# Optimization experiments

Hardware: AMD Instinct MI355X
Metric: run time of the kernel (lower is better)

## Reference

```python
import jax, jax.numpy as jnp
import numpy as np

N, TAPS, DIMS = 100000, 32, 2
LR_W, LR_F, LR_S, LR_B = 1.0 / 2**4, 1.0 / 2**7, 0.0, 1.0 / 2**11
GRAD_MAX_W, GRAD_MAX_F = 30.0, 30.0
EPS = 1e-8
BETA = 0.0  # commplax ddlms default: fshat <- f * s each step


def qam16_const():
    a = np.array([-3.0, -1.0, 1.0, 3.0], dtype=np.float32)
    re, im = np.meshgrid(a, a)
    c = (re + 1j * im).reshape(-1).astype(np.complex64)
    c = c / np.sqrt(np.mean(np.abs(c) ** 2))  # unit average power (/= sqrt(10))
    return jnp.asarray(c, dtype=jnp.complex64)


def mimo(w, u):
    # w: [dims, dims, taps], u: [taps, dims] -> [dims]
    return jnp.einsum('ijt,tj->i', w, u)


def setup_inputs() -> dict:
    key = jax.random.key(0)
    framed_signal_ri = jax.random.normal(key, (N, TAPS, DIMS, 2), dtype=jnp.float32)
    return {"framed_signal_ri": framed_signal_ri}


def reference(framed_signal_ri):
    u_all = (framed_signal_ri[..., 0] + 1j * framed_signal_ri[..., 1]).astype(jnp.complex64)  # [N, taps, dims]
    const = qam16_const()

    w0 = jnp.zeros((DIMS, DIMS, TAPS), jnp.complex64)
    f0 = jnp.ones((DIMS,), jnp.complex64)
    s0 = jnp.ones((DIMS,), jnp.complex64)
    b0 = jnp.zeros((DIMS,), jnp.complex64)
    fshat0 = jnp.ones((DIMS,), jnp.complex64)

    def clip_cmplx(g, gmax):
        # |g|<=gmax: unchanged; else g/|g|*gmax. Safe form (no div-by-zero).
        return g * (gmax / jnp.maximum(jnp.abs(g), gmax))

    def step(carry, u):
        w, f, s, b, fshat = carry
        v = mimo(w, u)                 # [dims]
        k = v * f
        c = k * s
        z = c + b
        q = v * fshat + b
        # decision-directed symbol (train=False)
        d = jax.lax.stop_gradient(const[jnp.argmin(jnp.abs(const[:, None] - q[None, :]), axis=0)])
        l = jnp.sum(jnp.abs(z - d) ** 2)

        psi_hat = jnp.abs(f) / f * jnp.abs(s) / s
        e_w = (d - b) * psi_hat - v
        e_f = d - b - k
        e_s = d - b - c
        e_b = d - z
        gw = (-1.0 / (jnp.sum(jnp.abs(u) ** 2) + EPS)) * e_w[:, None, None] * jnp.conj(u).T[None, ...]
        gf = (-1.0 / (jnp.abs(v) ** 2 + EPS)) * e_f * jnp.conj(v)
        gs = (-1.0 / (jnp.abs(k) ** 2 + EPS)) * e_s * jnp.conj(k)
        gb = -e_b

        gw = clip_cmplx(gw, GRAD_MAX_W)
        gf = clip_cmplx(gf, GRAD_MAX_F)

        out = ((w, f, s, b), l)  # weights used at this step + loss

        w = w - LR_W * gw
        f = f - LR_F * gf
        s = s - LR_S * gs
        b = b - LR_B * gb
        fshat = BETA * fshat + (1.0 - BETA) * (f * s)
        return (w, f, s, b, fshat), out

    _, ((ws, fs, ss, bs), ls) = jax.lax.scan(step, (w0, f0, s0, b0, fshat0), u_all)
    # apply: per-step equalization with the step's weights
    signal = jax.vmap(mimo)(ws, u_all) * fs * ss + bs   # [N, dims] complex64
    # emit as real/imag float32 pair for harness comparability
    return jnp.stack([jnp.real(signal), jnp.imag(signal)], axis=-1)
```

## Files before the change

kernel.cpp:

```cpp
#include <hip/hip_runtime.h>

#define N_STEPS 100000
#define NDIMS 2
#define ELEMS 64
#define LR_W 0.0625f
#define LR_F 0.0078125f
#define LR_B 0.00048828125f
#define GMAXF 30.0f
#define EPS_C 1e-8f
#define C_HALF_S10 1.58113883f
#define INV_S10 0.316227766f
#define TWO_INV_S10 0.6324555320f

#define DPPADD(v, ctrl, rmask)                                                   \
    do {                                                                         \
        int _t = __builtin_amdgcn_update_dpp(0, __float_as_int(v), ctrl, rmask,  \
                                             0xF, true);                         \
        (v) += __int_as_float(_t);                                               \
    } while (0)

__device__ inline float allsum64(float x) {
    x += __shfl_xor(x, 1);
    x += __shfl_xor(x, 2);
    x += __shfl_xor(x, 4);
    x += __shfl_xor(x, 8);
    x += __shfl_xor(x, 16);
    x += __shfl_xor(x, 32);
    return x;
}

__global__ __launch_bounds__(256) void ddlms_pre(const float2* __restrict__ u,
                                                 float4* __restrict__ C,
                                                 float2* __restrict__ D) {
    const int wave = threadIdx.x >> 6;
    const int lane = threadIdx.x & 63;
    const int n = blockIdx.x * 4 + wave;
    if (n >= N_STEPS) return;
    const int n1 = min(n + 1, N_STEPS - 1);
    const int n2 = min(n + 2, N_STEPS - 1);
    float2 u0 = u[(size_t)n  * ELEMS + lane];
    float2 u1 = u[(size_t)n1 * ELEMS + lane];
    float2 u2 = u[(size_t)n2 * ELEMS + lane];
    float su  = u0.x * u0.x + u0.y * u0.y;
    float r1r = u0.x * u1.x + u0.y * u1.y;
    float r1i = u0.x * u1.y - u0.y * u1.x;
    float r2r = u0.x * u2.x + u0.y * u2.y;
    float r2i = u0.x * u2.y - u0.y * u2.x;
    su  = allsum64(su);
    r1r = allsum64(r1r);
    r1i = allsum64(r1i);
    r2r = allsum64(r2r);
    r2i = allsum64(r2i);
    if (lane == 0) {
        float kappa = LR_W / (su + EPS_C);
        C[n] = make_float4(kappa, kappa * r1r, kappa * r1i, 0.0f);
        D[n] = make_float2(kappa * r2r, kappa * r2i);
    }
}

__global__ __launch_bounds__(64, 1) void ddlms_main(const float2* __restrict__ uin,
                                                    const float4* __restrict__ C,
                                                    const float2* __restrict__ D,
                                                    float2* __restrict__ out) {
    const int dim  = blockIdx.x;
    const int lane = threadIdx.x;

    float wr = 0.0f, wi = 0.0f;
    float vr = 0.0f, vi = 0.0f;
    float fr = 1.0f, fi = 0.0f;
    float br = 0.0f, bi = 0.0f;
    float psir = 1.0f, psii = 0.0f;
    float fs2r = C_HALF_S10, fs2i = 0.0f;
    float bs2r = 0.0f, bs2i = 0.0f;
    float nbr = -INV_S10, nbi = -INV_S10;
    float redr = 0.0f, redi = 0.0f;
    float vpr = 0.0f, vpi = 0.0f;

    float2 ubuf[8];
    float2 uc = uin[lane];
#pragma unroll
    for (int k = 1; k <= 8; ++k)
        ubuf[k & 7] = uin[(size_t)k * ELEMS + lane];

    float4 creg[4];
    float2 dreg[4];
#pragma unroll
    for (int k = 0; k < 4; ++k) {
        creg[k] = C[k];
        dreg[k] = D[k];
    }

    float2 zbuf[8];
    float2* outp = out + dim;

    for (int nb = 0; nb < N_STEPS; nb += 8) {
#pragma unroll
        for (int q = 0; q < 8; ++q) {
            const int n = nb + q;

            const float kap = creg[q & 3].x;
            const float k1r = creg[q & 3].y;
            const float k1i = creg[q & 3].z;
            const float k2r = dreg[q & 3].x;
            const float k2i = dreg[q & 3].y;
            {
                const int cn = min(n + 4, N_STEPS - 1);
                creg[q & 3] = C[cn];
                dreg[q & 3] = D[cn];
            }

            float P2r = redr, P2i = redi;
            DPPADD(P2r, 0x140, 0xF); DPPADD(P2i, 0x140, 0xF);
            DPPADD(P2r, 0x142, 0xA); DPPADD(P2i, 0x142, 0xA);
            DPPADD(P2r, 0x143, 0xC); DPPADD(P2i, 0x143, 0xC);
            const float sP2r = __int_as_float(__builtin_amdgcn_readlane(__float_as_int(P2r), 63));
            const float sP2i = __int_as_float(__builtin_amdgcn_readlane(__float_as_int(P2i), 63));

            const float2 u2 = ubuf[(q + 2) & 7];
            float pr = fmaf(wr, u2.x, -wi * u2.y);
            float pi = fmaf(wr, u2.y,  wi * u2.x);
            DPPADD(pr, 0xB1, 0xF);  DPPADD(pi, 0xB1, 0xF);
            DPPADD(pr, 0x4E, 0xF);  DPPADD(pi, 0x4E, 0xF);
            DPPADD(pr, 0x141, 0xF); DPPADD(pi, 0x141, 0xF);

            const float2 un = ubuf[(q + 1) & 7];
            ubuf[(q + 1) & 7] = uin[(size_t)min(n + 9, N_STEPS - 1) * ELEMS + lane];

            const float m2v  = fmaf(vr, vr, vi * vi);
            const float me   = m2v + EPS_C;
            const float invv = __builtin_amdgcn_rcpf(me);
            const float LFi  = LR_F * invv;
            const float Gme  = GMAXF * me;

            const float zr = fmaf(vr, fr, fmaf(-vi, fi, br));
            const float zi = fmaf(vr, fi, fmaf( vi, fr, bi));
            zbuf[q] = make_float2(zr, zi);

            const float zsr = fmaf(vr, fs2r, fmaf(-vi, fs2i, bs2r));
            const float zsi = fmaf(vr, fs2i, fmaf( vi, fs2r, bs2i));
            const float mr = __builtin_amdgcn_fmed3f(ceilf(zsr), -1.0f, 2.0f);
            const float mi = __builtin_amdgcn_fmed3f(ceilf(zsi), -1.0f, 2.0f);

            const float dbr = fmaf(TWO_INV_S10, mr, nbr);
            const float dbi = fmaf(TWO_INV_S10, mi, nbi);
            const float er  = fmaf(TWO_INV_S10, mr, -(INV_S10 + zr));
            const float ei  = fmaf(TWO_INV_S10, mi, -(INV_S10 + zi));

            const float ewr = fmaf(dbr, psir, fmaf(-dbi, psii, -vr));
            const float ewi = fmaf(dbr, psii, fmaf( dbi, psir, -vi));

            const float baser = sP2r + vpr;
            const float basei = sP2i + vpi;
            const float vnr = fmaf(k1r, ewr, fmaf(-k1i, ewi, baser));
            const float vni = fmaf(k1r, ewi, fmaf( k1i, ewr, basei));

            vpr = fmaf(k2r, ewr, -k2i * ewi);
            vpi = fmaf(k2r, ewi,  k2i * ewr);

            const float mwr = kap * ewr, mwi = kap * ewi;
            wr = fmaf(mwr, uc.x, fmaf( mwi, uc.y, wr));
            wi = fmaf(mwi, uc.x, fmaf(-mwr, uc.y, wi));

            const float e2  = fmaf(er, er, ei * ei);
            const float rs  = __builtin_amdgcn_rsqf(e2 * m2v);
            const float fac = fminf(1.0f, Gme * rs);
            const float s   = LFi * fac;
            const float ecvr = fmaf(er, vr,  ei * vi);
            const float ecvi = fmaf(ei, vr, -er * vi);
            fr = fmaf(s, ecvr, fr);
            fi = fmaf(s, ecvi, fi);

            br = fmaf(LR_B, er, br);
            bi = fmaf(LR_B, ei, bi);

            const float m2f = fmaf(fr, fr, fi * fi);
            const float rsf = __builtin_amdgcn_rsqf(m2f);
            psir = fr * rsf;
            psii = -fi * rsf;

            fs2r = C_HALF_S10 * fr; fs2i = C_HALF_S10 * fi;
            bs2r = C_HALF_S10 * br; bs2i = C_HALF_S10 * bi;
            nbr = -(INV_S10 + br);  nbi = -(INV_S10 + bi);

            vr = vnr; vi = vni;
            uc = un;
            redr = pr; redi = pi;
        }

        if (lane == 0) {
#pragma unroll
            for (int q = 0; q < 8; ++q)
                outp[(size_t)(nb + q) * NDIMS] = zbuf[q];
        }
    }
}

extern "C" void kernel_launch(void* const* d_in, const int* in_sizes, int n_in,
                              void* d_out, int out_size, void* d_ws, size_t ws_size,
                              hipStream_t stream) {
    const float2* u = (const float2*)d_in[0];
    float4* C = (float4*)d_ws;
    float2* D = (float2*)((char*)d_ws + (size_t)N_STEPS * sizeof(float4));
    ddlms_pre<<<(N_STEPS + 3) / 4, 256, 0, stream>>>(u, C, D);
    ddlms_main<<<NDIMS, 64, 0, stream>>>(u, C, D, (float2*)d_out);
}
```

Before: 23.46 ms.

## Interleave per-step coefficients, deepen prefetch, and move full reduction off the critical path

Packs the per-step coefficient records into one interleaved 32-byte array and prefetches them eight steps ahead instead of four. The address is made to depend on a per-lane zero (derived from input data), which makes the loads per-lane vector loads rather than scalar loads. The complete wavefront reduction of the next step's partial product, including the readlane, is now finished in the same iteration as that product is formed. This takes it off the start of the next step's serial dependency chain. In exchange there are more prefetch registers and vector-memory traffic, and launch_bounds no longer requests one block.

```diff
diff --git a/kernel.cpp b/kernel.cpp
--- a/kernel.cpp
+++ b/kernel.cpp
@@ -30,8 +30,7 @@
 }
 
 __global__ __launch_bounds__(256) void ddlms_pre(const float2* __restrict__ u,
-                                                 float4* __restrict__ C,
-                                                 float2* __restrict__ D) {
+                                                 float4* __restrict__ K) {
     const int wave = threadIdx.x >> 6;
     const int lane = threadIdx.x & 63;
     const int n = blockIdx.x * 4 + wave;
@@ -53,17 +52,20 @@
     r2i = allsum64(r2i);
     if (lane == 0) {
         float kappa = LR_W / (su + EPS_C);
-        C[n] = make_float4(kappa, kappa * r1r, kappa * r1i, 0.0f);
-        D[n] = make_float2(kappa * r2r, kappa * r2i);
+        K[2 * n]     = make_float4(kappa, kappa * r1r, kappa * r1i, 0.0f);
+        K[2 * n + 1] = make_float4(kappa * r2r, kappa * r2i, 0.0f, 0.0f);
     }
 }
 
-__global__ __launch_bounds__(64, 1) void ddlms_main(const float2* __restrict__ uin,
-                                                    const float4* __restrict__ C,
-                                                    const float2* __restrict__ D,
-                                                    float2* __restrict__ out) {
+__global__ __launch_bounds__(64) void ddlms_main(const float2* __restrict__ uin,
+                                                 const float4* __restrict__ K,
+                                                 float2* __restrict__ out) {
     const int dim  = blockIdx.x;
     const int lane = threadIdx.x;
+
+    const int ozero = (int)(uin[lane].x * 0.0f);
+    const char* Kc = (const char*)K;
+    const int koff = 32 * ozero;
 
     float wr = 0.0f, wi = 0.0f;
     float vr = 0.0f, vi = 0.0f;
@@ -73,7 +75,7 @@
     float fs2r = C_HALF_S10, fs2i = 0.0f;
     float bs2r = 0.0f, bs2i = 0.0f;
     float nbr = -INV_S10, nbi = -INV_S10;
-    float redr = 0.0f, redi = 0.0f;
+    float sPr = 0.0f, sPi = 0.0f;
     float vpr = 0.0f, vpi = 0.0f;
 
     float2 ubuf[8];
@@ -82,12 +84,12 @@
     for (int k = 1; k <= 8; ++k)
         ubuf[k & 7] = uin[(size_t)k * ELEMS + lane];
 
-    float4 creg[4];
-    float2 dreg[4];
-#pragma unroll
-    for (int k = 0; k < 4; ++k) {
-        creg[k] = C[k];
-        dreg[k] = D[k];
+    float4 kr1[8];
+    float2 kr2[8];
+#pragma unroll
+    for (int k = 0; k < 8; ++k) {
+        kr1[k] = *(const float4*)(Kc + 32 * k + koff);
+        kr2[k] = *(const float2*)(Kc + 32 * k + 16 + koff);
     }
 
     float2 zbuf[8];
@@ -98,23 +100,16 @@
         for (int q = 0; q < 8; ++q) {
             const int n = nb + q;
 
-            const float kap = creg[q & 3].x;
-            const float k1r = creg[q & 3].y;
-            const float k1i = creg[q & 3].z;
-            const float k2r = dreg[q & 3].x;
-            const float k2i = dreg[q & 3].y;
+            const float kap = kr1[q].x;
+            const float k1r = kr1[q].y;
+            const float k1i = kr1[q].z;
+            const float k2r = kr2[q].x;
+            const float k2i = kr2[q].y;
             {
-                const int cn = min(n + 4, N_STEPS - 1);
-                creg[q & 3] = C[cn];
-                dreg[q & 3] = D[cn];
+                const int cn = min(n + 8, N_STEPS - 1);
+                kr1[q] = *(const float4*)(Kc + 32 * cn + koff);
+                kr2[q] = *(const float2*)(Kc + 32 * cn + 16 + koff);
             }
-
-            float P2r = redr, P2i = redi;
-            DPPADD(P2r, 0x140, 0xF); DPPADD(P2i, 0x140, 0xF);
-            DPPADD(P2r, 0x142, 0xA); DPPADD(P2i, 0x142, 0xA);
-            DPPADD(P2r, 0x143, 0xC); DPPADD(P2i, 0x143, 0xC);
-            const float sP2r = __int_as_float(__builtin_amdgcn_readlane(__float_as_int(P2r), 63));
-            const float sP2i = __int_as_float(__builtin_amdgcn_readlane(__float_as_int(P2i), 63));
 
             const float2 u2 = ubuf[(q + 2) & 7];
             float pr = fmaf(wr, u2.x, -wi * u2.y);
@@ -122,6 +117,11 @@
             DPPADD(pr, 0xB1, 0xF);  DPPADD(pi, 0xB1, 0xF);
             DPPADD(pr, 0x4E, 0xF);  DPPADD(pi, 0x4E, 0xF);
             DPPADD(pr, 0x141, 0xF); DPPADD(pi, 0x141, 0xF);
+            DPPADD(pr, 0x140, 0xF); DPPADD(pi, 0x140, 0xF);
+            DPPADD(pr, 0x142, 0xA); DPPADD(pi, 0x142, 0xA);
+            DPPADD(pr, 0x143, 0xC); DPPADD(pi, 0x143, 0xC);
+            const float sPnr = __int_as_float(__builtin_amdgcn_readlane(__float_as_int(pr), 63));
+            const float sPni = __int_as_float(__builtin_amdgcn_readlane(__float_as_int(pi), 63));
 
             const float2 un = ubuf[(q + 1) & 7];
             ubuf[(q + 1) & 7] = uin[(size_t)min(n + 9, N_STEPS - 1) * ELEMS + lane];
@@ -149,8 +149,8 @@
             const float ewr = fmaf(dbr, psir, fmaf(-dbi, psii, -vr));
             const float ewi = fmaf(dbr, psii, fmaf( dbi, psir, -vi));
 
-            const float baser = sP2r + vpr;
-            const float basei = sP2i + vpi;
+            const float baser = sPr + vpr;
+            const float basei = sPi + vpi;
             const float vnr = fmaf(k1r, ewr, fmaf(-k1i, ewi, baser));
             const float vni = fmaf(k1r, ewi, fmaf( k1i, ewr, basei));
 
@@ -183,8 +183,8 @@
             nbr = -(INV_S10 + br);  nbi = -(INV_S10 + bi);
 
             vr = vnr; vi = vni;
+            sPr = sPnr; sPi = sPni;
             uc = un;
-            redr = pr; redi = pi;
         }
 
         if (lane == 0) {
@@ -199,8 +199,7 @@
                               void* d_out, int out_size, void* d_ws, size_t ws_size,
                               hipStream_t stream) {
     const float2* u = (const float2*)d_in[0];
-    float4* C = (float4*)d_ws;
-    float2* D = (float2*)((char*)d_ws + (size_t)N_STEPS * sizeof(float4));
-    ddlms_pre<<<(N_STEPS + 3) / 4, 256, 0, stream>>>(u, C, D);
-    ddlms_main<<<NDIMS, 64, 0, stream>>>(u, C, D, (float2*)d_out);
-}
+    float4* K = (float4*)d_ws;
+    ddlms_pre<<<(N_STEPS + 3) / 4, 256, 0, stream>>>(u, K);
+    ddlms_main<<<NDIMS, 64, 0, stream>>>(u, K, (float2*)d_out);
+}
```

Measured after the change: 21.69 ms. 1.08x faster.
